# Optimization experiments

Measured on AMD Instinct MI355X. Metric: run time of the kernel, lower is better.

The kernel has to match this reference:

```python
import jax, jax.numpy as jnp
import numpy as np

ADAPTER_RATIO = 0.2


def setup_inputs() -> dict:
    key = jax.random.key(0)
    k1, k2, k3, k4, k5 = jax.random.split(key, 5)
    B, D, R, N_DOM, N_TXT = 16384, 1024, 256, 3, 1380
    image_features = jax.random.normal(k1, (B, D), dtype=jnp.float32)
    domain_labels = jax.random.randint(k2, (B,), 0, N_DOM, dtype=jnp.int64)
    W1 = jax.random.normal(k3, (N_DOM, D, R), dtype=jnp.float32) * 0.02
    W2 = jax.random.normal(k4, (N_DOM, R, D), dtype=jnp.float32) * 0.02
    txt = jax.random.normal(k5, (N_TXT, D), dtype=jnp.float32)
    # text features are L2-normalized at module init (encode_text then norm)
    text_features = txt / jnp.linalg.norm(txt, axis=-1, keepdims=True)
    logit_scale = jnp.asarray(np.log(1.0 / 0.07), dtype=jnp.float32)  # CLIP init
    return {
        "image_features": image_features,
        "domain_labels": domain_labels,
        "W1": W1,
        "W2": W2,
        "text_features": text_features,
        "logit_scale": logit_scale,
    }


def reference(image_features, domain_labels, W1, W2, text_features, logit_scale):
    # Domain-routed adapter MLP: run all n_domains experts (n is tiny), then
    # select the routed output per sample (equivalent to the per-sample loop).
    h = jax.nn.relu(jnp.einsum("bd,ndr->bnr", image_features, W1))  # [B,n,R]
    a = jax.nn.relu(jnp.einsum("bnr,nrd->bnd", h, W2))              # [B,n,D]
    idx = domain_labels[:, None, None]                                # [B,1,1]
    adapter_features = jnp.take_along_axis(a, idx, axis=1)[:, 0, :]   # [B,D]
    fused = ADAPTER_RATIO * adapter_features + (1.0 - ADAPTER_RATIO) * image_features
    fused = fused / jnp.linalg.norm(fused, axis=-1, keepdims=True)
    # text_features already normalized; concat over domains done upstream: [N_TXT, D]
    logits = jnp.exp(logit_scale) * (fused @ text_features.T)         # [B, N_TXT]
    return logits
```

## Files before the change

kernel.cpp:

```cpp
#include <hip/hip_runtime.h>
#include <hip/hip_bf16.h>
#include <math.h>

using bf16 = __hip_bfloat16;
typedef __attribute__((ext_vector_type(8))) short bf16x8;
typedef __attribute__((ext_vector_type(4))) float f32x4;
typedef __attribute__((ext_vector_type(4))) unsigned short us4;

#define GAS __attribute__((address_space(1)))
#define LAS __attribute__((address_space(3)))

__device__ __forceinline__ void gload_lds16(const bf16* g, bf16* lds) {
  __builtin_amdgcn_global_load_lds((const GAS void*)g, (LAS void*)lds, 16, 0, 0);
}
__device__ __forceinline__ float b2f(unsigned short u) {
  union { unsigned short s; bf16 b; } x; x.s = u; return __bfloat162float(x.b);
}

__global__ __launch_bounds__(256) void hist_k(const int* __restrict__ lab,
                                              int* __restrict__ blockHist) {
  const int blk = blockIdx.x, t = threadIdx.x;
  const int lane = t & 63, w = t >> 6;
  const int d = lab[blk * 256 + t];
  __shared__ int wc[4][3];
#pragma unroll
  for (int dd = 0; dd < 3; ++dd) {
    unsigned long long m = __ballot(d == dd);
    if (lane == 0) wc[w][dd] = __popcll(m);
  }
  __syncthreads();
  if (t < 3) blockHist[blk * 3 + t] = wc[0][t] + wc[1][t] + wc[2][t] + wc[3][t];
}

__global__ __launch_bounds__(256) void scan_k(const int* __restrict__ blockHist,
                                              int* __restrict__ blockOff,
                                              int* __restrict__ meta) {
  __shared__ int h[64][3];
  __shared__ int tot[3];
  const int t = threadIdx.x;
  if (t < 192) h[t / 3][t % 3] = blockHist[t];
  __syncthreads();
  if (t < 3) {
    int s = 0;
    for (int b = 0; b < 64; ++b) { int v = h[b][t]; h[b][t] = s; s += v; }
    tot[t] = s;
    meta[t] = s;
  }
  __syncthreads();
  if (t == 0) { meta[4] = 0; meta[5] = tot[0]; meta[6] = tot[0] + tot[1]; }
  if (t < 192) {
    int b = t / 3, d = t % 3;
    int base = (d == 0) ? 0 : (d == 1 ? tot[0] : tot[0] + tot[1]);
    blockOff[t] = base + h[b][d];
  }
}

__global__ __launch_bounds__(256) void scatter2_k(const int* __restrict__ lab,
                                                  const int* __restrict__ blockOff,
                                                  int* __restrict__ perm,
                                                  int* __restrict__ iperm) {
  const int blk = blockIdx.x, t = threadIdx.x;
  const int lane = t & 63, w = t >> 6;
  const int i = blk * 256 + t;
  const int d = lab[i];
  __shared__ int wc[4][3];
  unsigned long long mymask = 0;
#pragma unroll
  for (int dd = 0; dd < 3; ++dd) {
    unsigned long long m = __ballot(d == dd);
    if (lane == 0) wc[w][dd] = __popcll(m);
    if (dd == d) mymask = m;
  }
  __syncthreads();
  int woff = 0;
  for (int ww = 0; ww < w; ++ww) woff += wc[ww][d];
  const unsigned long long lt = ((unsigned long long)1 << lane) - 1;
  const int rank = blockOff[blk * 3 + d] + woff + __popcll(mymask & lt);
  perm[rank] = i;
  iperm[i] = rank;
}

__global__ __launch_bounds__(256) void cvt_all_k(const float* __restrict__ x,
                                                 const float* __restrict__ W1,
                                                 const float* __restrict__ W2,
                                                 const float* __restrict__ txt,
                                                 const int* __restrict__ iperm,
                                                 bf16* __restrict__ Xbc,
                                                 bf16* __restrict__ W1T,
                                                 bf16* __restrict__ W2T,
                                                 bf16* __restrict__ Tb) {
  const int nx = 16384 * 1024 / 4;
  const int n1 = 3 * 256 * 1024;
  const int n2 = n1 + 3 * 1024 * 256;
  const int n3 = n2 + 1536 * 1024;
  const int total = nx + n3;
  for (int i = blockIdx.x * 256 + threadIdx.x; i < total; i += 4096 * 256) {
    if (i < nx) {
      const int row = i >> 8, c4 = i & 255;
      float4 v = ((const float4*)x)[i];
      bf16 t[4] = {__float2bfloat16(v.x), __float2bfloat16(v.y),
                   __float2bfloat16(v.z), __float2bfloat16(v.w)};
      ((us4*)Xbc)[(size_t)iperm[row] * 256 + c4] = *(const us4*)t;
      continue;
    }
    int j = i - nx;
    if (j < n1) {
      int d = j >> 18, rem = j & 262143;
      int r = rem >> 10, k = rem & 1023;
      W1T[j] = __float2bfloat16(W1[(size_t)d * 262144 + (size_t)k * 256 + r]);
    } else if (j < n2) {
      int jj = j - n1;
      int d = jj >> 18, rem = jj & 262143;
      int n = rem >> 8, k = rem & 255;
      W2T[jj] = __float2bfloat16(W2[(size_t)d * 262144 + (size_t)k * 1024 + n]);
    } else {
      int jj = j - n2;
      Tb[jj] = (jj < 1380 * 1024) ? __float2bfloat16(txt[jj]) : __float2bfloat16(0.f);
    }
  }
}

template <int EPI, int NBLK>
__global__ __launch_bounds__(256) void gemm_bt(
    const bf16* __restrict__ A, const bf16* __restrict__ BT, bf16* __restrict__ Cv,
    const int* __restrict__ meta, int N, int K, int ldc, int Nvalid,
    const bf16* __restrict__ xb, float* __restrict__ ssp) {
  const int bid = blockIdx.x;
  const int xcd = bid & 7;
  const int seq = bid >> 3;
  const int nblkidx = seq % NBLK;
  const int dm = xcd + 8 * (seq / NBLK);
  const int dom = dm >> 7;
  const int mblk = dm & 127;

  const int cnt = meta[dom];
  const int base = meta[4 + dom];
  BT += (size_t)dom * N * K;

  const int m0 = mblk * 128;
  if (m0 >= cnt) return;
  const int n0 = nblkidx * 128;

  __shared__ bf16 sA[2][128][32];
  __shared__ bf16 sB[2][128][32];

  const int tid = threadIdx.x;
  const int wid = tid >> 6;
  const int lane = tid & 63;

  const int srow = (wid << 4) + (lane >> 2);
  const int skoff = (((lane & 3) ^ ((lane >> 2) & 3)) << 3);

  int p0 = m0 + srow;       if (p0 > cnt - 1) p0 = cnt - 1;
  int p1 = m0 + srow + 64;  if (p1 > cnt - 1) p1 = cnt - 1;
  const bf16* a0 = A + (size_t)(base + p0) * K + skoff;
  const bf16* a1 = A + (size_t)(base + p1) * K + skoff;
  const bf16* b0 = BT + (size_t)(n0 + srow) * K + skoff;
  const bf16* b1 = BT + (size_t)(n0 + srow + 64) * K + skoff;

  const int fr = lane & 15;
  const int fq = lane >> 4;
  const int rchunk = (fq ^ (fr & 3)) << 3;

  f32x4 acc[4][4];
#pragma unroll
  for (int m = 0; m < 4; ++m)
#pragma unroll
    for (int n = 0; n < 4; ++n) acc[m][n] = (f32x4){0.f, 0.f, 0.f, 0.f};

  const int nk = K >> 5;
  auto stage = [&](int buf, int kt) {
    gload_lds16(a0 + kt * 32, &sA[buf][wid * 16][0]);
    gload_lds16(a1 + kt * 32, &sA[buf][wid * 16 + 64][0]);
    gload_lds16(b0 + kt * 32, &sB[buf][wid * 16][0]);
    gload_lds16(b1 + kt * 32, &sB[buf][wid * 16 + 64][0]);
  };

  stage(0, 0);
  __syncthreads();
  const int wr = wid >> 1, wc = wid & 1;
  for (int kt = 0; kt < nk; ++kt) {
    const int cur = kt & 1;
    if (kt + 1 < nk) stage(cur ^ 1, kt + 1);
    bf16x8 af[4], bfr[4];
#pragma unroll
    for (int m = 0; m < 4; ++m)
      af[m] = *(const bf16x8*)&sA[cur][wr * 64 + m * 16 + fr][rchunk];
#pragma unroll
    for (int n = 0; n < 4; ++n)
      bfr[n] = *(const bf16x8*)&sB[cur][wc * 64 + n * 16 + fr][rchunk];
#pragma unroll
    for (int m = 0; m < 4; ++m)
#pragma unroll
      for (int n = 0; n < 4; ++n)
        acc[m][n] = __builtin_amdgcn_mfma_f32_16x16x32_bf16(af[m], bfr[n], acc[m][n], 0, 0, 0);
    __syncthreads();
  }

  if (EPI == 0) {
#pragma unroll
    for (int m = 0; m < 4; ++m) {
#pragma unroll
      for (int r = 0; r < 4; ++r) {
        const int p = m0 + wr * 64 + m * 16 + fq * 4 + r;
        if (p < cnt) {
          const size_t crow = (size_t)(base + p);
#pragma unroll
          for (int n = 0; n < 4; ++n) {
            const int col = n0 + wc * 64 + n * 16 + fr;
            if (col < Nvalid)
              Cv[crow * (size_t)ldc + col] = __float2bfloat16(fmaxf(acc[m][n][r], 0.f));
          }
        }
      }
    }
  } else {
    __shared__ float ssred[128][2];
#pragma unroll
    for (int m = 0; m < 4; ++m) {
#pragma unroll
      for (int r = 0; r < 4; ++r) {
        const int lr = wr * 64 + m * 16 + fq * 4 + r;
        const int p = m0 + lr;
        float rowss = 0.f;
        if (p < cnt) {
          const size_t crow = (size_t)(base + p);
#pragma unroll
          for (int n = 0; n < 4; ++n) {
            const int col = n0 + wc * 64 + n * 16 + fr;
            const float g = 0.2f * fmaxf(acc[m][n][r], 0.f) +
                            0.8f * b2f(*(const unsigned short*)&xb[crow * 1024 + col]);
            Cv[crow * (size_t)ldc + col] = __float2bfloat16(g);
            rowss += g * g;
          }
        }
        rowss += __shfl_xor(rowss, 1, 16);
        rowss += __shfl_xor(rowss, 2, 16);
        rowss += __shfl_xor(rowss, 4, 16);
        rowss += __shfl_xor(rowss, 8, 16);
        if (fr == 0) ssred[lr][wc] = rowss;
      }
    }
    __syncthreads();
    if (tid < 128) {
      const int p = m0 + tid;
      if (p < cnt)
        ssp[(size_t)nblkidx * 16384 + base + p] = ssred[tid][0] + ssred[tid][1];
    }
  }
}

__global__ __launch_bounds__(256, 2) void gemm3_occ(
    const bf16* __restrict__ A, const bf16* __restrict__ BT,
    float* __restrict__ C, const float* __restrict__ scale_ptr,
    const float* __restrict__ ssp, const int* __restrict__ perm) {
  extern __shared__ bf16 smem[];
  bf16* sA0 = smem;
  bf16* sB0 = smem + 16384;

  const int tid = threadIdx.x;
  const int lane = tid & 63, wid = tid >> 6;
  const int wr = wid >> 1, wc = wid & 1;
  const int fr = lane & 15, fq = lane >> 4;

  const int bid = blockIdx.x;
  const int x = bid & 7, seq = bid >> 3;
  const int mb = x * 16 + (seq >> 3), nb = seq & 7;
  const int m0 = mb << 7, n0 = nb * 192;

  auto STAGE = [&](int t) {
    const int s = t & 1, koff = t << 6;
    bf16* da = sA0 + (s << 13);
#pragma unroll
    for (int L = 0; L < 4; ++L) {
      const int idx = (L << 8) + tid;
      const int r = idx >> 3, c = idx & 7;
      gload_lds16(A + (size_t)(m0 + r) * 1024 + koff + ((c ^ (r & 7)) << 3),
                  da + ((idx & ~63) << 3));
    }
    bf16* db = sB0 + s * 12288;
#pragma unroll
    for (int L = 0; L < 6; ++L) {
      const int idx = (L << 8) + tid;
      const int r = idx >> 3, c = idx & 7;
      gload_lds16(BT + (size_t)(n0 + r) * 1024 + koff + ((c ^ (r & 7)) << 3),
                  db + ((idx & ~63) << 3));
    }
  };
  auto LDA = [&](int s, int kk, bf16x8* dst) {
    const bf16* base = sA0 + (s << 13);
#pragma unroll
    for (int m = 0; m < 4; ++m) {
      const int row = (wr << 6) + (m << 4) + fr;
      dst[m] = *(const bf16x8*)(base + (row << 6) + ((((kk << 2) + fq) ^ (fr & 7)) << 3));
    }
  };
  auto LDB = [&](int s, int kk, bf16x8* dst) {
    const bf16* base = sB0 + s * 12288;
#pragma unroll
    for (int n = 0; n < 6; ++n) {
      const int row = wc * 96 + (n << 4) + fr;
      dst[n] = *(const bf16x8*)(base + (row << 6) + ((((kk << 2) + fq) ^ (fr & 7)) << 3));
    }
  };

  f32x4 acc[4][6];
#pragma unroll
  for (int m = 0; m < 4; ++m)
#pragma unroll
    for (int n = 0; n < 6; ++n) acc[m][n] = (f32x4){0.f, 0.f, 0.f, 0.f};

  STAGE(0);
  __syncthreads();
  const int nt = 16;
  for (int t = 0; t < nt; ++t) {
    const int s = t & 1;
    if (t + 1 < nt) STAGE(t + 1);
    bf16x8 a0[4], a1[4], b0[6], b1[6];
    LDA(s, 0, a0); LDB(s, 0, b0);
    LDA(s, 1, a1); LDB(s, 1, b1);
#pragma unroll
    for (int m = 0; m < 4; ++m)
#pragma unroll
      for (int n = 0; n < 6; ++n)
        acc[m][n] = __builtin_amdgcn_mfma_f32_16x16x32_bf16(a0[m], b0[n], acc[m][n], 0, 0, 0);
#pragma unroll
    for (int m = 0; m < 4; ++m)
#pragma unroll
      for (int n = 0; n < 6; ++n)
        acc[m][n] = __builtin_amdgcn_mfma_f32_16x16x32_bf16(a1[m], b1[n], acc[m][n], 0, 0, 0);
    __syncthreads();
  }

  float* rlds = (float*)smem;
  int*   plds = (int*)((char*)smem + 512);
  if (tid < 128) {
    float s = 0.f;
#pragma unroll
    for (int b = 0; b < 8; ++b) s += ssp[b * 16384 + m0 + tid];
    rlds[tid] = rsqrtf(s);
    plds[tid] = perm[m0 + tid];
  }
  __syncthreads();

  const float sc = expf(*scale_ptr);
#pragma unroll
  for (int m = 0; m < 4; ++m) {
    const int lrow = (wr << 6) + (m << 4) + (fq << 2);
#pragma unroll
    for (int r = 0; r < 4; ++r) {
      const float rv = sc * rlds[lrow + r];
      const size_t orow = (size_t)plds[lrow + r];
#pragma unroll
      for (int n = 0; n < 6; ++n) {
        const int gcol = n0 + wc * 96 + (n << 4) + fr;
        if (gcol < 1380) C[orow * 1380 + gcol] = acc[m][n][r] * rv;
      }
    }
  }
}

extern "C" void kernel_launch(void* const* d_in, const int* in_sizes, int n_in,
                              void* d_out, int out_size, void* d_ws, size_t ws_size,
                              hipStream_t stream) {
  (void)in_sizes; (void)n_in; (void)out_size; (void)ws_size;
  const float* x    = (const float*)d_in[0];
  const int*   lab  = (const int*)d_in[1];
  const float* W1   = (const float*)d_in[2];
  const float* W2   = (const float*)d_in[3];
  const float* text = (const float*)d_in[4];
  const float* lsc  = (const float*)d_in[5];
  float* out = (float*)d_out;

  const int B = 16384, D = 1024, R = 256, NTP = 1536;

  char* p = (char*)d_ws;
  auto carve = [&](size_t bytes) {
    char* r = p;
    p += (bytes + 255) & ~(size_t)255;
    return r;
  };
  int*   meta  = (int*)carve(64);
  int*   bhist = (int*)carve(64 * 3 * 4);
  int*   boff  = (int*)carve(64 * 3 * 4);
  int*   perm  = (int*)carve((size_t)B * 4);
  int*   iperm = (int*)carve((size_t)B * 4);
  float* ssp   = (float*)carve((size_t)8 * B * 4);
  bf16*  Xbc   = (bf16*)carve((size_t)B * D * 2);
  bf16*  W1T   = (bf16*)carve((size_t)3 * R * D * 2);
  bf16*  W2T   = (bf16*)carve((size_t)3 * D * R * 2);
  bf16*  Tb    = (bf16*)carve((size_t)NTP * D * 2);
  bf16*  H     = (bf16*)carve((size_t)B * R * 2);
  bf16*  Fbc   = (bf16*)carve((size_t)B * D * 2);

  hist_k<<<B / 256, 256, 0, stream>>>(lab, bhist);
  scan_k<<<1, 256, 0, stream>>>(bhist, boff, meta);
  scatter2_k<<<B / 256, 256, 0, stream>>>(lab, boff, perm, iperm);

  cvt_all_k<<<4096, 256, 0, stream>>>(x, W1, W2, text, iperm, Xbc, W1T, W2T, Tb);

  gemm_bt<0, 2><<<768, 256, 0, stream>>>(
      Xbc, W1T, H, meta, R, D, R, R, nullptr, nullptr);
  gemm_bt<1, 8><<<3072, 256, 0, stream>>>(
      H, W2T, Fbc, meta, D, R, D, D, Xbc, ssp);
  gemm3_occ<<<1024, 256, 81920, stream>>>(Fbc, Tb, out, lsc, ssp, perm);
}
```

Before: 160.4 us.

## Split weight transpose into tiled kernel and deepen gemm3 prefetch pipeline

Moves W1/W2 transpose-to-bf16 out of the strided conversion loop into a dedicated 64x64 LDS-tiled transpose kernel so reads and writes are coalesced. The final GEMM now issues loads two stages ahead, gating on explicit vmcnt/lgkmcnt waits with raw barriers and raising wave priority around the MFMA block. This aims to reduce exposed global-load latency and uncoalesced weight reads, at the cost of an extra launch and hardcoded wait counts that depend on the per-stage load count.

```diff
diff --git a/kernel.cpp b/kernel.cpp
--- a/kernel.cpp
+++ b/kernel.cpp
@@ -81,43 +81,50 @@
 }
 
 __global__ __launch_bounds__(256) void cvt_all_k(const float* __restrict__ x,
-                                                 const float* __restrict__ W1,
-                                                 const float* __restrict__ W2,
                                                  const float* __restrict__ txt,
                                                  const int* __restrict__ iperm,
                                                  bf16* __restrict__ Xbc,
-                                                 bf16* __restrict__ W1T,
-                                                 bf16* __restrict__ W2T,
                                                  bf16* __restrict__ Tb) {
   const int nx = 16384 * 1024 / 4;
-  const int n1 = 3 * 256 * 1024;
-  const int n2 = n1 + 3 * 1024 * 256;
-  const int n3 = n2 + 1536 * 1024;
-  const int total = nx + n3;
-  for (int i = blockIdx.x * 256 + threadIdx.x; i < total; i += 4096 * 256) {
+  const int ntext = 1536 * 1024;
+  const int total = nx + ntext;
+  for (int i = blockIdx.x * 256 + threadIdx.x; i < total; i += 2048 * 256) {
     if (i < nx) {
       const int row = i >> 8, c4 = i & 255;
       float4 v = ((const float4*)x)[i];
       bf16 t[4] = {__float2bfloat16(v.x), __float2bfloat16(v.y),
                    __float2bfloat16(v.z), __float2bfloat16(v.w)};
       ((us4*)Xbc)[(size_t)iperm[row] * 256 + c4] = *(const us4*)t;
-      continue;
-    }
-    int j = i - nx;
-    if (j < n1) {
-      int d = j >> 18, rem = j & 262143;
-      int r = rem >> 10, k = rem & 1023;
-      W1T[j] = __float2bfloat16(W1[(size_t)d * 262144 + (size_t)k * 256 + r]);
-    } else if (j < n2) {
-      int jj = j - n1;
-      int d = jj >> 18, rem = jj & 262143;
-      int n = rem >> 8, k = rem & 255;
-      W2T[jj] = __float2bfloat16(W2[(size_t)d * 262144 + (size_t)k * 1024 + n]);
     } else {
-      int jj = j - n2;
+      int jj = i - nx;
       Tb[jj] = (jj < 1380 * 1024) ? __float2bfloat16(txt[jj]) : __float2bfloat16(0.f);
     }
   }
+}
+
+__global__ __launch_bounds__(256) void tr_wt_k(const float* __restrict__ W1,
+                                               const float* __restrict__ W2,
+                                               bf16* __restrict__ W1T,
+                                               bf16* __restrict__ W2T) {
+  __shared__ float s[64][65];
+  int b = blockIdx.x;
+  const float* W; bf16* WT; int R, C;
+  if (b < 192) { W = W1; WT = W1T; R = 1024; C = 256; }
+  else         { b -= 192; W = W2; WT = W2T; R = 256; C = 1024; }
+  const int d = b / 64, tb = b % 64;
+  const int tilesPerRow = C / 64;
+  const int r0 = (tb / tilesPerRow) * 64;
+  const int c0 = (tb % tilesPerRow) * 64;
+  const float* Wd = W + (size_t)d * R * C;
+  bf16* WTd = WT + (size_t)d * R * C;
+  const int tx = threadIdx.x & 63, ty = threadIdx.x >> 6;
+#pragma unroll
+  for (int i = 0; i < 16; ++i)
+    s[ty + i * 4][tx] = Wd[(size_t)(r0 + ty + i * 4) * C + c0 + tx];
+  __syncthreads();
+#pragma unroll
+  for (int i = 0; i < 16; ++i)
+    WTd[(size_t)(c0 + ty + i * 4) * R + r0 + tx] = __float2bfloat16(s[tx][ty + i * 4]);
 }
 
 template <int EPI, int NBLK>
@@ -250,7 +257,7 @@
   }
 }
 
-__global__ __launch_bounds__(256, 2) void gemm3_occ(
+__global__ __launch_bounds__(256, 2) void gemm3_cnt(
     const bf16* __restrict__ A, const bf16* __restrict__ BT,
     float* __restrict__ C, const float* __restrict__ scale_ptr,
     const float* __restrict__ ssp, const int* __restrict__ perm) {
@@ -310,15 +317,22 @@
 #pragma unroll
     for (int n = 0; n < 6; ++n) acc[m][n] = (f32x4){0.f, 0.f, 0.f, 0.f};
 
-  STAGE(0);
-  __syncthreads();
+  STAGE(0); STAGE(1);
+  asm volatile("s_waitcnt vmcnt(10)" ::: "memory");
+  __builtin_amdgcn_s_barrier();
+
   const int nt = 16;
   for (int t = 0; t < nt; ++t) {
     const int s = t & 1;
-    if (t + 1 < nt) STAGE(t + 1);
     bf16x8 a0[4], a1[4], b0[6], b1[6];
     LDA(s, 0, a0); LDB(s, 0, b0);
     LDA(s, 1, a1); LDB(s, 1, b1);
+    asm volatile("s_waitcnt lgkmcnt(0)" ::: "memory");
+    __builtin_amdgcn_sched_barrier(0);
+    __builtin_amdgcn_s_barrier();
+    __builtin_amdgcn_sched_barrier(0);
+    if (t + 2 < nt) STAGE(t + 2);
+    __builtin_amdgcn_s_setprio(1);
 #pragma unroll
     for (int m = 0; m < 4; ++m)
 #pragma unroll
@@ -329,7 +343,15 @@
 #pragma unroll
       for (int n = 0; n < 6; ++n)
         acc[m][n] = __builtin_amdgcn_mfma_f32_16x16x32_bf16(a1[m], b1[n], acc[m][n], 0, 0, 0);
-    __syncthreads();
+    __builtin_amdgcn_s_setprio(0);
+    if (t + 2 < nt) {
+      asm volatile("s_waitcnt vmcnt(10)" ::: "memory");
+    } else if (t + 1 < nt) {
+      asm volatile("s_waitcnt vmcnt(0)" ::: "memory");
+    }
+    __builtin_amdgcn_sched_barrier(0);
+    __builtin_amdgcn_s_barrier();
+    __builtin_amdgcn_sched_barrier(0);
   }
 
   float* rlds = (float*)smem;
@@ -397,11 +419,12 @@
   scan_k<<<1, 256, 0, stream>>>(bhist, boff, meta);
   scatter2_k<<<B / 256, 256, 0, stream>>>(lab, boff, perm, iperm);
 
-  cvt_all_k<<<4096, 256, 0, stream>>>(x, W1, W2, text, iperm, Xbc, W1T, W2T, Tb);
+  cvt_all_k<<<2048, 256, 0, stream>>>(x, text, iperm, Xbc, Tb);
+  tr_wt_k<<<384, 256, 0, stream>>>(W1, W2, W1T, W2T);
 
   gemm_bt<0, 2><<<768, 256, 0, stream>>>(
       Xbc, W1T, H, meta, R, D, R, R, nullptr, nullptr);
   gemm_bt<1, 8><<<3072, 256, 0, stream>>>(
       H, W2T, Fbc, meta, D, R, D, D, Xbc, ssp);
-  gemm3_occ<<<1024, 256, 81920, stream>>>(Fbc, Tb, out, lsc, ssp, perm);
-}
+  gemm3_cnt<<<1024, 256, 81920, stream>>>(Fbc, Tb, out, lsc, ssp, perm);
+}
```

New measurement: 154.5 us. -3.7%, faster.
